# Optimization experiments

Measured on AMD Instinct MI355X. Metric: run time of the kernel, lower is better.

## Reference

```python
import jax, jax.numpy as jnp
import numpy as np

N_TOKEN = 392
POS_WEIGHT = 1.0
LOSS_WEIGHT = 1.0


def _cam_map(logits, w_proj, xf, shape):
    # logits: (B, K_cls); w_proj: (K_cls, C); xf: (B, C, N)
    B, T, H, W = shape
    top_cls = jnp.argmax(logits, axis=1)                 # sort desc -> [0] == argmax
    w_top = w_proj[top_cls]                              # (B, C) gather top-class weight row
    row = jnp.einsum('bc,bcn->bn', w_top, xf)            # (B, N) per-sample CAM scores
    mn = row.min(axis=1, keepdims=True)
    mx = row.max(axis=1, keepdims=True)
    rown = (row - mn) / (mx - mn)                        # min-max normalize
    vals, idxs = jax.lax.top_k(rown, N_TOKEN)            # (B, 392)
    hw = H * W
    ti = idxs // hw
    hi = (idxs % hw) // W
    wi = idxs % W
    bi = jnp.broadcast_to(jnp.arange(B)[:, None], idxs.shape)
    cam = jnp.zeros((B, T, H, W), rown.dtype).at[bi, ti, hi, wi].set(vals)
    return cam


def _forward(x, pred_v_logits, pred_n_logits, w_proj_v, w_proj_n,
             conv_w, conv_b, score_w, score_b):
    B, C, T, H, W = x.shape
    xf = x.reshape(B, C, T * H * W)
    cam_v = _cam_map(pred_v_logits, w_proj_v, xf, (B, T, H, W))
    cam_n = _cam_map(pred_n_logits, w_proj_n, xf, (B, T, H, W))
    cam_gt = jnp.maximum(cam_v, cam_n)                   # torch.where(v > n, v, n)
    cam_gt = jax.lax.stop_gradient(cam_gt)               # original builds it from numpy + .detach()

    dn = ('NCDHW', 'OIDHW', 'NCDHW')
    h1 = jax.nn.relu(
        jax.lax.conv_general_dilated(x, conv_w, (1, 1, 1),
                                     [(0, 0), (1, 1), (1, 1)],
                                     dimension_numbers=dn)
        + conv_b[None, :, None, None, None])
    logits = (jax.lax.conv_general_dilated(h1, score_w, (1, 1, 1),
                                           [(0, 0), (0, 0), (0, 0)],
                                           dimension_numbers=dn)
              + score_b[None, :, None, None, None])      # (B,1,T,H,W)

    xcam = logits[:, 0].reshape(B * T, H * W)
    y = cam_gt.reshape(B * T, H * W)
    # BCEWithLogitsLoss(pos_weight) mean
    bce = -(POS_WEIGHT * y * jax.nn.log_sigmoid(xcam)
            + (1.0 - y) * jax.nn.log_sigmoid(-xcam))
    return LOSS_WEIGHT * bce.mean()


def setup_inputs() -> dict:
    key = jax.random.key(0)
    ks = jax.random.split(key, 8)
    B, C, T, H, W = 64, 256, 32, 7, 7
    Kv, Kn, D = 97, 300, 512
    x = jax.random.normal(ks[0], (B, C, T, H, W), jnp.float32)
    pred_v_logits = jax.random.normal(ks[1], (B, Kv), jnp.float32)
    pred_n_logits = jax.random.normal(ks[2], (B, Kn), jnp.float32)
    w_proj_v = jax.random.normal(ks[3], (Kv, C), jnp.float32) / np.sqrt(C)
    w_proj_n = jax.random.normal(ks[4], (Kn, C), jnp.float32) / np.sqrt(C)
    conv_w = jax.random.normal(ks[5], (D, C, 1, 3, 3), jnp.float32) / np.sqrt(C * 9)
    conv_b = jnp.zeros((D,), jnp.float32)
    score_w = jax.random.normal(ks[6], (1, D, 1, 1, 1), jnp.float32) / np.sqrt(D)
    score_b = jnp.zeros((1,), jnp.float32)
    return {"x": x, "pred_v_logits": pred_v_logits, "pred_n_logits": pred_n_logits,
            "w_proj_v": w_proj_v, "w_proj_n": w_proj_n,
            "conv_w": conv_w, "conv_b": conv_b,
            "score_w": score_w, "score_b": score_b}


def reference(x, pred_v_logits, pred_n_logits, w_proj_v, w_proj_n,
              conv_w, conv_b, score_w, score_b):
    return _forward(x, pred_v_logits, pred_n_logits, w_proj_v, w_proj_n,
                    conv_w, conv_b, score_w, score_b)
```

## Files before the change

### kernel.cpp

```cpp
#include <hip/hip_runtime.h>
#include <hip/hip_bf16.h>
#include <math.h>

#define BB 64
#define CC 256
#define TT 32
#define HH 7
#define WW 7
#define HW 49
#define NN 1568
#define KV 97
#define KN 300
#define DD 512
#define NTOK 392
#define TOTAL (BB*TT*HW)
#define BCAP 256

typedef float f32x4 __attribute__((ext_vector_type(4)));
typedef short bf16x8 __attribute__((ext_vector_type(8)));

#define GLDS(g, l) __builtin_amdgcn_global_load_lds(                          \
    (const __attribute__((address_space(1))) void*)(g),                       \
    (__attribute__((address_space(3))) void*)(l), 16, 0, 0)

__global__ __launch_bounds__(256) void k_tr(
        const float* __restrict__ x, __hip_bfloat16* __restrict__ xp,
        const float* __restrict__ cw, __hip_bfloat16* __restrict__ wb,
        int* __restrict__ counter) {
    __shared__ float xs[392 * 33];
    int bid = blockIdx.x;
    int tid = threadIdx.x;
    if (bid == 0 && tid == 0) *counter = 0;

    {
        int base = bid * 576;
        #pragma unroll
        for (int r = 0; r < 3; ++r) {
            int o = base + r * 256 + tid;
            if (o < base + 576) {
                int kk = o / (DD * CC);
                int rem = o - kk * (DD * CC);
                int d = rem >> 8, c = rem & 255;
                wb[o] = __float2bfloat16(cw[(d * CC + c) * 9 + kk]);
            }
        }
    }

    int b  = bid >> 5;
    int cc = (bid >> 2) & 7;
    int tc = bid & 3;
    int c0 = cc << 5;
    int t0 = tc << 3;

    const float* xbase = x + ((size_t)((b * CC + c0) * TT + t0)) * HW;
    const float4* xb4 = (const float4*)xbase;
    for (int base = 0; base < 3072; base += 1024) {
        float4 v[4]; int li[4];
        #pragma unroll
        for (int j = 0; j < 4; ++j) {
            int idx = base + j * 256 + tid;
            v[j] = xb4[idx];
            int ch = idx / 98, o4 = idx - ch * 98;
            li[j] = (o4 * 4) * 33 + ch;
        }
        #pragma unroll
        for (int j = 0; j < 4; ++j) {
            xs[li[j]     ] = v[j].x;
            xs[li[j] + 33] = v[j].y;
            xs[li[j] + 66] = v[j].z;
            xs[li[j] + 99] = v[j].w;
        }
    }
    {
        int idx = 3072 + tid;
        if (idx < 3136) {
            float4 v = xb4[idx];
            int ch = idx / 98, o4 = idx - ch * 98;
            int li = (o4 * 4) * 33 + ch;
            xs[li] = v.x; xs[li + 33] = v.y; xs[li + 66] = v.z; xs[li + 99] = v.w;
        }
    }
    __syncthreads();

    __hip_bfloat16* xpb = xp + ((size_t)(b * TT + t0) * 81) * 256 + c0;
    for (int u = tid; u < 2592; u += 256) {
        int pos = u >> 2, cq = u & 3;
        int tt = pos / 81, p = pos - tt * 81;
        int hh = p / 9, ww = p - (p / 9) * 9;
        bool inb = (hh >= 1 && hh <= 7 && ww >= 1 && ww <= 7);
        const float* row = xs + (tt * 49 + (hh - 1) * 7 + (ww - 1)) * 33 + cq * 8;
        bf16x8 pack;
        #pragma unroll
        for (int j = 0; j < 8; ++j) {
            float v = inb ? row[j] : 0.f;
            __hip_bfloat16 bv = __float2bfloat16(v);
            pack[j] = *reinterpret_cast<short*>(&bv);
        }
        *reinterpret_cast<bf16x8*>(xpb + (size_t)(tt * 81 + p) * 256 + cq * 8) = pack;
    }
}

__device__ __forceinline__ int binof(float v) {
    int i = (int)(v * 1024.f);
    return i < 0 ? 0 : (i > 1023 ? 1023 : i);
}

__device__ void cam_block(int b, int tid, char* smem,
                          const float* __restrict__ x,
                          const float* __restrict__ pv, const float* __restrict__ pn,
                          const float* __restrict__ wpv, const float* __restrict__ wpn,
                          float* __restrict__ cam) {
    float* rv = (float*)smem;
    float* rn = (float*)(smem + 6272);
    int* h = (int*)(smem + 12544);
    int* tsum = (int*)(smem + 16640);
    float* lval_v = (float*)(smem + 17664);
    int* lidx_v = (int*)(smem + 18688);
    float* lval_n = (float*)(smem + 19712);
    int* lidx_n = (int*)(smem + 20736);
    float* wred = (float*)(smem + 21760);
    int* sc = (int*)(smem + 21824);
    float* wvs = (float*)(smem + 21888);
    float* wns = (float*)(smem + 22912);
    int* cls2 = (int*)(smem + 23936);

    int lane = tid & 63;
    if (tid < 128) {
        int head = tid >> 6;
        const float* r = head ? (pn + b * KN) : (pv + b * KV);
        int K = head ? KN : KV;
        float best = -1e30f; int bi = 0x7fffffff;
        for (int k = lane; k < K; k += 64) {
            float v = r[k];
            if (v > best || (v == best && k < bi)) { best = v; bi = k; }
        }
        #pragma unroll
        for (int off = 32; off >= 1; off >>= 1) {
            float ov = __shfl_xor(best, off);
            int oi = __shfl_xor(bi, off);
            if (ov > best || (ov == best && oi < bi)) { best = ov; bi = oi; }
        }
        if (lane == 0) cls2[head] = bi;
    }
    __syncthreads();
    wvs[tid] = wpv[cls2[0] * CC + tid];
    wns[tid] = wpn[cls2[1] * CC + tid];
    __syncthreads();

    {
        const f32x4* xb4 = (const f32x4*)(x + (size_t)b * CC * NN);
        bool two = tid < (392 - 256);
        f32x4 av0 = {0.f,0.f,0.f,0.f}, an0 = {0.f,0.f,0.f,0.f};
        f32x4 av1 = {0.f,0.f,0.f,0.f}, an1 = {0.f,0.f,0.f,0.f};
        for (int c = 0; c < CC; ++c) {
            float wv = wvs[c], wn = wns[c];
            const f32x4* rowc = xb4 + (size_t)c * 392;
            f32x4 u0 = rowc[tid];
            #pragma unroll
            for (int r = 0; r < 4; ++r) {
                av0[r] = fmaf(wv, u0[r], av0[r]);
                an0[r] = fmaf(wn, u0[r], an0[r]);
            }
            if (two) {
                f32x4 u1 = rowc[tid + 256];
                #pragma unroll
                for (int r = 0; r < 4; ++r) {
                    av1[r] = fmaf(wv, u1[r], av1[r]);
                    an1[r] = fmaf(wn, u1[r], an1[r]);
                }
            }
        }
        *reinterpret_cast<f32x4*>(rv + 4 * tid) = av0;
        *reinterpret_cast<f32x4*>(rn + 4 * tid) = an0;
        if (two) {
            *reinterpret_cast<f32x4*>(rv + 4 * (tid + 256)) = av1;
            *reinterpret_cast<f32x4*>(rn + 4 * (tid + 256)) = an1;
        }
    }
    __syncthreads();

    float mnv = 1e30f, mxv = -1e30f, mnn = 1e30f, mxn = -1e30f;
    for (int n = tid; n < NN; n += 256) {
        float v = rv[n]; mnv = fminf(mnv, v); mxv = fmaxf(mxv, v);
        float u = rn[n]; mnn = fminf(mnn, u); mxn = fmaxf(mxn, u);
    }
    #pragma unroll
    for (int off = 32; off >= 1; off >>= 1) {
        mnv = fminf(mnv, __shfl_xor(mnv, off));
        mxv = fmaxf(mxv, __shfl_xor(mxv, off));
        mnn = fminf(mnn, __shfl_xor(mnn, off));
        mxn = fmaxf(mxn, __shfl_xor(mxn, off));
    }
    if ((tid & 63) == 0) {
        int wid = tid >> 6;
        wred[wid * 4 + 0] = mnv; wred[wid * 4 + 1] = mxv;
        wred[wid * 4 + 2] = mnn; wred[wid * 4 + 3] = mxn;
    }
    if (tid == 0) { sc[0] = 0; sc[1] = 0; }
    __syncthreads();
    mnv = fminf(fminf(wred[0], wred[4]), fminf(wred[8], wred[12]));
    mxv = fmaxf(fmaxf(wred[1], wred[5]), fmaxf(wred[9], wred[13]));
    mnn = fminf(fminf(wred[2], wred[6]), fminf(wred[10], wred[14]));
    mxn = fmaxf(fmaxf(wred[3], wred[7]), fmaxf(wred[11], wred[15]));
    float iv = 1.f / (mxv - mnv), inn = 1.f / (mxn - mnn);

    for (int n = tid; n < NN; n += 256) {
        rv[n] = (rv[n] - mnv) * iv;
        rn[n] = (rn[n] - mnn) * inn;
    }
    for (int i = tid; i < 1024; i += 256) h[i] = 0;
    __syncthreads();
    for (int n = tid; n < NN; n += 256) {
        atomicAdd(&h[binof(rv[n])], 1);
        atomicAdd(&h[binof(rn[n])], 1 << 16);
    }
    __syncthreads();

    int h0 = h[4 * tid], h1 = h[4 * tid + 1], h2 = h[4 * tid + 2], h3 = h[4 * tid + 3];
    tsum[tid] = h0 + h1 + h2 + h3;
    __syncthreads();
    for (int off = 1; off < 256; off <<= 1) {
        int add = (tid + off < 256) ? tsum[tid + off] : 0;
        __syncthreads();
        tsum[tid] += add;
        __syncthreads();
    }
    {
        int scur = tsum[tid];
        int hk[4] = {h0, h1, h2, h3};
        #pragma unroll
        for (int k = 0; k < 4; ++k) {
            int snext = scur - hk[k];
            int scv = scur & 0xffff, ncv = snext & 0xffff;
            int sh = scur >> 16, nh = snext >> 16;
            if (scv >= NTOK && ncv < NTOK) { sc[2] = 4 * tid + k; sc[3] = ncv; }
            if (sh >= NTOK && nh < NTOK) { sc[4] = 4 * tid + k; sc[5] = nh; }
            scur = snext;
        }
    }
    __syncthreads();
    int bsv = sc[2], abv = sc[3], bsn = sc[4], abn = sc[5];

    for (int n = tid; n < NN; n += 256) {
        float v = rv[n]; int bv = binof(v);
        if (bv < bsv) rv[n] = 0.f;
        else if (bv == bsv) {
            int s = atomicAdd(&sc[0], 1);
            if (s < BCAP) { lval_v[s] = v; lidx_v[s] = n; }
        }
        float u = rn[n]; int bu = binof(u);
        if (bu < bsn) rn[n] = 0.f;
        else if (bu == bsn) {
            int s = atomicAdd(&sc[1], 1);
            if (s < BCAP) { lval_n[s] = u; lidx_n[s] = n; }
        }
    }
    __syncthreads();
    int Lv = sc[0] < BCAP ? sc[0] : BCAP;
    int Ln = sc[1] < BCAP ? sc[1] : BCAP;
    for (int i = tid; i < Lv; i += 256) {
        float vi = lval_v[i]; int ni = lidx_v[i]; int r = 0;
        for (int j = 0; j < Lv; ++j) {
            float vj = lval_v[j]; int nj = lidx_v[j];
            r += (vj > vi || (vj == vi && nj < ni)) ? 1 : 0;
        }
        rv[ni] = (r < NTOK - abv) ? vi : 0.f;
    }
    for (int i = tid; i < Ln; i += 256) {
        float vi = lval_n[i]; int ni = lidx_n[i]; int r = 0;
        for (int j = 0; j < Ln; ++j) {
            float vj = lval_n[j]; int nj = lidx_n[j];
            r += (vj > vi || (vj == vi && nj < ni)) ? 1 : 0;
        }
        rn[ni] = (r < NTOK - abn) ? vi : 0.f;
    }
    __syncthreads();
    for (int n = tid; n < NN; n += 256) cam[b * NN + n] = fmaxf(rv[n], rn[n]);
}

__global__ __launch_bounds__(256, 3) void k_gemm(
        const __hip_bfloat16* __restrict__ xp, const __hip_bfloat16* __restrict__ wb,
        const float* __restrict__ convb, const float* __restrict__ scorew,
        float* __restrict__ pl,
        const float* __restrict__ x,
        const float* __restrict__ pv, const float* __restrict__ pn,
        const float* __restrict__ wpv, const float* __restrict__ wpn,
        float* __restrict__ cam) {
    __shared__ char smem[32768];
    int tid = threadIdx.x;
    int bid = blockIdx.x;
    if (bid < 64) { cam_block(bid, tid, smem, x, pv, pn, wpv, wpn, cam); return; }
    char* As = smem;
    char* Bs = smem + 16384;
    int gid = bid - 64;
    int xcd = gid & 7;
    int local = gid >> 3;
    int mtile = xcd * 98 + (local >> 2);
    int nblk = local & 3;
    int m0 = mtile * 128;
    int n0 = nblk * 128;
    int lane = tid & 63, wv = tid >> 6;
    int wm = wv >> 1, wn = wv & 1;
    int ln = lane & 15, qd = lane >> 4;

    int rrow = tid >> 3;
    int segst = ((tid & 7) ^ (rrow & 7)) * 8;
    int bt_[4], hh_[4], ww_[4];
    const __hip_bfloat16* bptr[4];
    #pragma unroll
    for (int j = 0; j < 4; ++j) {
        int m = m0 + j * 32 + rrow;
        int bt = m / HW, q = m - bt * HW;
        bt_[j] = bt; hh_[j] = q / WW; ww_[j] = q - (q / WW) * WW;
        bptr[j] = wb + (size_t)(n0 + j * 32 + rrow) * 256 + segst;
    }

    int swz = ln & 7;
    int offk[2] = {((0 + qd) ^ swz) * 16, ((4 + qd) ^ swz) * 16};

    f32x4 acc[4][4];
    #pragma unroll
    for (int i = 0; i < 4; ++i)
        #pragma unroll
        for (int j = 0; j < 4; ++j) acc[i][j] = (f32x4){0.f, 0.f, 0.f, 0.f};

    for (int kk = 0; kk < 9; ++kk) {
        int kh = kk / 3, kw = kk - (kk / 3) * 3;
        const __hip_bfloat16* aptr[4];
        #pragma unroll
        for (int j = 0; j < 4; ++j)
            aptr[j] = xp + ((size_t)bt_[j] * 81 + (hh_[j] + kh) * 9 + (ww_[j] + kw)) * 256 + segst;
        const size_t boff = (size_t)kk * (DD * 256);
        #pragma unroll
        for (int c0 = 0; c0 < 256; c0 += 64) {
            __syncthreads();
            #pragma unroll
            for (int j = 0; j < 4; ++j) {
                GLDS(aptr[j] + c0, As + j * 4096 + tid * 16);
                GLDS(bptr[j] + boff + c0, Bs + j * 4096 + tid * 16);
            }
            __syncthreads();
            #pragma unroll
            for (int k2 = 0; k2 < 2; ++k2) {
                bf16x8 af[4], bfr[4];
                #pragma unroll
                for (int i = 0; i < 4; ++i)
                    af[i] = *(const bf16x8*)(As + (wm * 64 + i * 16 + ln) * 128 + offk[k2]);
                #pragma unroll
                for (int j = 0; j < 4; ++j)
                    bfr[j] = *(const bf16x8*)(Bs + (wn * 64 + j * 16 + ln) * 128 + offk[k2]);
                #pragma unroll
                for (int i = 0; i < 4; ++i)
                    #pragma unroll
                    for (int j = 0; j < 4; ++j)
                        acc[i][j] = __builtin_amdgcn_mfma_f32_16x16x32_bf16(af[i], bfr[j], acc[i][j], 0, 0, 0);
            }
        }
    }

    float swr[4], cbr[4];
    #pragma unroll
    for (int j = 0; j < 4; ++j) {
        int n = n0 + wn * 64 + j * 16 + ln;
        swr[j] = scorew[n];
        cbr[j] = convb[n];
    }
    float* dst = pl + (size_t)(nblk * 2 + wn) * TOTAL;
    #pragma unroll
    for (int i = 0; i < 4; ++i) {
        #pragma unroll
        for (int r = 0; r < 4; ++r) {
            float v = 0.f;
            #pragma unroll
            for (int j = 0; j < 4; ++j) {
                float h1 = acc[i][j][r] + cbr[j];
                h1 = h1 > 0.f ? h1 : 0.f;
                v = fmaf(swr[j], h1, v);
            }
            v += __shfl_xor(v, 1);
            v += __shfl_xor(v, 2);
            v += __shfl_xor(v, 4);
            v += __shfl_xor(v, 8);
            if (ln == 0)
                dst[m0 + wm * 64 + i * 16 + qd * 4 + r] = v;
        }
    }
}

__global__ __launch_bounds__(256) void k_bce(
        const float* __restrict__ pl, const float* __restrict__ cam,
        const float* __restrict__ sb, float* __restrict__ part,
        int* __restrict__ counter, float* __restrict__ out) {
    __shared__ float sbuf[256];
    __shared__ int isLast;
    int tid = threadIdx.x;
    int m = blockIdx.x * 256 + tid;
    float l = sb[0];
    #pragma unroll
    for (int s = 0; s < 8; ++s) l += pl[(size_t)s * TOTAL + m];
    float y = cam[m];
    float v = fmaxf(l, 0.f) - l * y + log1pf(expf(-fabsf(l)));
    sbuf[tid] = v; __syncthreads();
    for (int k = 128; k > 0; k >>= 1) {
        if (tid < k) sbuf[tid] += sbuf[tid + k];
        __syncthreads();
    }
    if (tid == 0) {
        part[blockIdx.x] = sbuf[0];
        __threadfence();
        int d = atomicAdd(counter, 1);
        isLast = (d == 391);
    }
    __syncthreads();
    if (isLast) {
        float s = 0.f;
        for (int i = tid; i < 392; i += 256) s += part[i];
        sbuf[tid] = s; __syncthreads();
        for (int k = 128; k > 0; k >>= 1) {
            if (tid < k) sbuf[tid] += sbuf[tid + k];
            __syncthreads();
        }
        if (tid == 0) out[0] = sbuf[0] * (1.0f / (float)TOTAL);
    }
}

extern "C" void kernel_launch(void* const* d_in, const int* in_sizes, int n_in,
                              void* d_out, int out_size, void* d_ws, size_t ws_size,
                              hipStream_t stream) {
    const float* x   = (const float*)d_in[0];
    const float* pv  = (const float*)d_in[1];
    const float* pn  = (const float*)d_in[2];
    const float* wpv = (const float*)d_in[3];
    const float* wpn = (const float*)d_in[4];
    const float* cw  = (const float*)d_in[5];
    const float* cb  = (const float*)d_in[6];
    const float* sw  = (const float*)d_in[7];
    const float* sb  = (const float*)d_in[8];

    char* w8 = (char*)d_ws;
    __hip_bfloat16* xp  = (__hip_bfloat16*)w8;
    __hip_bfloat16* wb  = (__hip_bfloat16*)(w8 + 84934656);
    float* pl      = (float*)(w8 + 87293952);
    float* cam     = (float*)(w8 + 90505216);
    float* part    = (float*)(w8 + 90906624);
    int*   counter = (int*)(w8 + 90908192);

    k_tr<<<2048, 256, 0, stream>>>(x, xp, cw, wb, counter);
    k_gemm<<<64 + 3136, 256, 0, stream>>>(xp, wb, cb, sw, pl,
                                          x, pv, pn, wpv, wpn, cam);
    k_bce<<<392, 256, 0, stream>>>(pl, cam, sb, part, counter, (float*)d_out);
}
```

Baseline: 411.6 us.

## Double-buffer LDS tiles to overlap global loads with MFMA compute

Restructures the conv-GEMM main loop into 36 flattened stages that use two 32KB LDS buffers. The next stage's global_load_lds is issued before computing on the current buffer, and partial vmcnt waits let the loads overlap the MFMA work. LDS doubles to 64KB and launch bounds drop to 2 blocks per SM, so occupancy falls in exchange for the overlap. It also relies on hand-placed s_barrier and waitcnt assembly, which may be fragile.

```diff
diff --git a/kernel.cpp b/kernel.cpp
--- a/kernel.cpp
+++ b/kernel.cpp
@@ -278,7 +278,7 @@
     for (int n = tid; n < NN; n += 256) cam[b * NN + n] = fmaxf(rv[n], rn[n]);
 }
 
-__global__ __launch_bounds__(256, 3) void k_gemm(
+__global__ __launch_bounds__(256, 2) void k_gemm(
         const __hip_bfloat16* __restrict__ xp, const __hip_bfloat16* __restrict__ wb,
         const float* __restrict__ convb, const float* __restrict__ scorew,
         float* __restrict__ pl,
@@ -286,12 +286,10 @@
         const float* __restrict__ pv, const float* __restrict__ pn,
         const float* __restrict__ wpv, const float* __restrict__ wpn,
         float* __restrict__ cam) {
-    __shared__ char smem[32768];
+    __shared__ char smem[65536];
     int tid = threadIdx.x;
     int bid = blockIdx.x;
     if (bid < 64) { cam_block(bid, tid, smem, x, pv, pn, wpv, wpn, cam); return; }
-    char* As = smem;
-    char* Bs = smem + 16384;
     int gid = bid - 64;
     int xcd = gid & 7;
     int local = gid >> 3;
@@ -324,37 +322,49 @@
         #pragma unroll
         for (int j = 0; j < 4; ++j) acc[i][j] = (f32x4){0.f, 0.f, 0.f, 0.f};
 
-    for (int kk = 0; kk < 9; ++kk) {
-        int kh = kk / 3, kw = kk - (kk / 3) * 3;
-        const __hip_bfloat16* aptr[4];
-        #pragma unroll
-        for (int j = 0; j < 4; ++j)
-            aptr[j] = xp + ((size_t)bt_[j] * 81 + (hh_[j] + kh) * 9 + (ww_[j] + kw)) * 256 + segst;
-        const size_t boff = (size_t)kk * (DD * 256);
-        #pragma unroll
-        for (int c0 = 0; c0 < 256; c0 += 64) {
-            __syncthreads();
+    auto STAGE = [&](int s, int wbo) {
+        int kk = s >> 2;
+        int kh = kk / 3, kw = kk - kh * 3;
+        int c0 = (s & 3) << 6;
+        const size_t boff = (size_t)kk * (DD * 256) + c0;
+        #pragma unroll
+        for (int j = 0; j < 4; ++j) {
+            const __hip_bfloat16* ap = xp
+                + ((size_t)bt_[j] * 81 + (hh_[j] + kh) * 9 + (ww_[j] + kw)) * 256
+                + segst + c0;
+            GLDS(ap, smem + wbo + j * 4096 + tid * 16);
+            GLDS(bptr[j] + boff, smem + wbo + 16384 + j * 4096 + tid * 16);
+        }
+    };
+
+    STAGE(0, 0);
+    #pragma unroll 2
+    for (int s = 0; s < 36; ++s) {
+        int rb = (s & 1) << 15;
+        asm volatile("s_barrier" ::: "memory");
+        if (s < 35) {
+            STAGE(s + 1, ((s + 1) & 1) << 15);
+            asm volatile("s_waitcnt vmcnt(8)" ::: "memory");
+        } else {
+            asm volatile("s_waitcnt vmcnt(0)" ::: "memory");
+        }
+        asm volatile("s_barrier" ::: "memory");
+        const char* Asr = smem + rb;
+        const char* Bsr = smem + rb + 16384;
+        #pragma unroll
+        for (int k2 = 0; k2 < 2; ++k2) {
+            bf16x8 af[4], bfr[4];
             #pragma unroll
-            for (int j = 0; j < 4; ++j) {
-                GLDS(aptr[j] + c0, As + j * 4096 + tid * 16);
-                GLDS(bptr[j] + boff + c0, Bs + j * 4096 + tid * 16);
-            }
-            __syncthreads();
+            for (int i = 0; i < 4; ++i)
+                af[i] = *(const bf16x8*)(Asr + (wm * 64 + i * 16 + ln) * 128 + offk[k2]);
             #pragma unroll
-            for (int k2 = 0; k2 < 2; ++k2) {
-                bf16x8 af[4], bfr[4];
-                #pragma unroll
-                for (int i = 0; i < 4; ++i)
-                    af[i] = *(const bf16x8*)(As + (wm * 64 + i * 16 + ln) * 128 + offk[k2]);
+            for (int j = 0; j < 4; ++j)
+                bfr[j] = *(const bf16x8*)(Bsr + (wn * 64 + j * 16 + ln) * 128 + offk[k2]);
+            #pragma unroll
+            for (int i = 0; i < 4; ++i)
                 #pragma unroll
                 for (int j = 0; j < 4; ++j)
-                    bfr[j] = *(const bf16x8*)(Bs + (wn * 64 + j * 16 + ln) * 128 + offk[k2]);
-                #pragma unroll
-                for (int i = 0; i < 4; ++i)
-                    #pragma unroll
-                    for (int j = 0; j < 4; ++j)
-                        acc[i][j] = __builtin_amdgcn_mfma_f32_16x16x32_bf16(af[i], bfr[j], acc[i][j], 0, 0, 0);
-            }
+                    acc[i][j] = __builtin_amdgcn_mfma_f32_16x16x32_bf16(af[i], bfr[j], acc[i][j], 0, 0, 0);
         }
     }
 
```

Measured after the change: 430.6 us. 4.6% more time.

## Restructure padded-transpose kernel to cover all channels per block with bf16 staging

Applied to the files above, without the earlier changes.

The transpose/pad kernel now gives each block all 256 channels for two time steps instead of 32 channels by 8 time steps, and halves the grid. Each thread loads its own channel's contiguous float2 run and converts to bf16 before writing to LDS. The LDS tile shrinks and the padded output is written as fully contiguous 16-byte stores per position row. The weight-conversion loop is widened to match the smaller grid. The cost is that the global loads are now strided across threads, since each lane reads a separate channel row. Coalescing then relies on cache reuse across loop iterations.

```diff
diff --git a/kernel.cpp b/kernel.cpp
--- a/kernel.cpp
+++ b/kernel.cpp
@@ -23,21 +23,21 @@
     (const __attribute__((address_space(1))) void*)(g),                       \
     (__attribute__((address_space(3))) void*)(l), 16, 0, 0)
 
-__global__ __launch_bounds__(256) void k_tr(
+__global__ __launch_bounds__(256, 3) void k_tr(
         const float* __restrict__ x, __hip_bfloat16* __restrict__ xp,
         const float* __restrict__ cw, __hip_bfloat16* __restrict__ wb,
         int* __restrict__ counter) {
-    __shared__ float xs[392 * 33];
+    __shared__ unsigned short xs[98 * 256];
     int bid = blockIdx.x;
     int tid = threadIdx.x;
     if (bid == 0 && tid == 0) *counter = 0;
 
     {
-        int base = bid * 576;
-        #pragma unroll
-        for (int r = 0; r < 3; ++r) {
+        int base = bid * 1152;
+        #pragma unroll
+        for (int r = 0; r < 5; ++r) {
             int o = base + r * 256 + tid;
-            if (o < base + 576) {
+            if (o < base + 1152) {
                 int kk = o / (DD * CC);
                 int rem = o - kk * (DD * CC);
                 int d = rem >> 8, c = rem & 255;
@@ -46,57 +46,46 @@
         }
     }
 
-    int b  = bid >> 5;
-    int cc = (bid >> 2) & 7;
-    int tc = bid & 3;
-    int c0 = cc << 5;
-    int t0 = tc << 3;
-
-    const float* xbase = x + ((size_t)((b * CC + c0) * TT + t0)) * HW;
-    const float4* xb4 = (const float4*)xbase;
-    for (int base = 0; base < 3072; base += 1024) {
-        float4 v[4]; int li[4];
-        #pragma unroll
-        for (int j = 0; j < 4; ++j) {
-            int idx = base + j * 256 + tid;
-            v[j] = xb4[idx];
-            int ch = idx / 98, o4 = idx - ch * 98;
-            li[j] = (o4 * 4) * 33 + ch;
-        }
-        #pragma unroll
-        for (int j = 0; j < 4; ++j) {
-            xs[li[j]     ] = v[j].x;
-            xs[li[j] + 33] = v[j].y;
-            xs[li[j] + 66] = v[j].z;
-            xs[li[j] + 99] = v[j].w;
+    int b  = bid >> 4;
+    int tp = bid & 15;
+    int t0 = tp << 1;
+
+    const float2* src = (const float2*)(x + ((size_t)(b * CC + tid) * TT + t0) * HW);
+    #pragma unroll 1
+    for (int r = 0; r < 6; ++r) {
+        float2 v[8];
+        #pragma unroll
+        for (int j = 0; j < 8; ++j) v[j] = src[r * 8 + j];
+        #pragma unroll
+        for (int j = 0; j < 8; ++j) {
+            int q = (r * 8 + j) * 2;
+            __hip_bfloat16 b0 = __float2bfloat16(v[j].x);
+            __hip_bfloat16 b1 = __float2bfloat16(v[j].y);
+            xs[q * 256 + tid] = *reinterpret_cast<unsigned short*>(&b0);
+            xs[(q + 1) * 256 + tid] = *reinterpret_cast<unsigned short*>(&b1);
         }
     }
     {
-        int idx = 3072 + tid;
-        if (idx < 3136) {
-            float4 v = xb4[idx];
-            int ch = idx / 98, o4 = idx - ch * 98;
-            int li = (o4 * 4) * 33 + ch;
-            xs[li] = v.x; xs[li + 33] = v.y; xs[li + 66] = v.z; xs[li + 99] = v.w;
-        }
-    }
-    __syncthreads();
-
-    __hip_bfloat16* xpb = xp + ((size_t)(b * TT + t0) * 81) * 256 + c0;
-    for (int u = tid; u < 2592; u += 256) {
-        int pos = u >> 2, cq = u & 3;
-        int tt = pos / 81, p = pos - tt * 81;
+        float2 v = src[48];
+        __hip_bfloat16 b0 = __float2bfloat16(v.x);
+        __hip_bfloat16 b1 = __float2bfloat16(v.y);
+        xs[96 * 256 + tid] = *reinterpret_cast<unsigned short*>(&b0);
+        xs[97 * 256 + tid] = *reinterpret_cast<unsigned short*>(&b1);
+    }
+    __syncthreads();
+
+    __hip_bfloat16* xpb = xp + (size_t)(b * TT + t0) * 81 * 256;
+    const bf16x8 zero = (bf16x8){0, 0, 0, 0, 0, 0, 0, 0};
+    for (int u = tid; u < 5184; u += 256) {
+        int pos = u >> 5, c0 = (u & 31) * 8;
+        int f = pos / 81, p = pos - f * 81;
         int hh = p / 9, ww = p - (p / 9) * 9;
-        bool inb = (hh >= 1 && hh <= 7 && ww >= 1 && ww <= 7);
-        const float* row = xs + (tt * 49 + (hh - 1) * 7 + (ww - 1)) * 33 + cq * 8;
-        bf16x8 pack;
-        #pragma unroll
-        for (int j = 0; j < 8; ++j) {
-            float v = inb ? row[j] : 0.f;
-            __hip_bfloat16 bv = __float2bfloat16(v);
-            pack[j] = *reinterpret_cast<short*>(&bv);
-        }
-        *reinterpret_cast<bf16x8*>(xpb + (size_t)(tt * 81 + p) * 256 + cq * 8) = pack;
+        bf16x8 val = zero;
+        if (hh >= 1 && hh <= 7 && ww >= 1 && ww <= 7) {
+            int q = f * 49 + (hh - 1) * 7 + (ww - 1);
+            val = *reinterpret_cast<const bf16x8*>(xs + q * 256 + c0);
+        }
+        *reinterpret_cast<bf16x8*>(xpb + (size_t)u * 8) = val;
     }
 }
 
@@ -445,7 +434,7 @@
     float* part    = (float*)(w8 + 90906624);
     int*   counter = (int*)(w8 + 90908192);
 
-    k_tr<<<2048, 256, 0, stream>>>(x, xp, cw, wb, counter);
+    k_tr<<<1024, 256, 0, stream>>>(x, xp, cw, wb, counter);
     k_gemm<<<64 + 3136, 256, 0, stream>>>(xp, wb, cb, sw, pl,
                                           x, pv, pn, wpv, wpn, cam);
     k_bce<<<392, 256, 0, stream>>>(pl, cam, sb, part, counter, (float*)d_out);
```

Result: slower. 432.7 us (+5.1%).

## Drop padded halo from bf16 activation copy and redirect halo loads to zero buffer

Applied to the files above, without the earlier changes.

The transpose kernel now writes the bf16 channels-last activation without the 9x9 zero-padded halo, which cuts the intermediate buffer from 81 to 49 positions per frame and shrinks write traffic. The implicit-GEMM kernel computes the halo condition per row and points halo loads at a small zeroed buffer that the transpose kernel initializes. Separately, the CAM dot-product loop is unrolled by four channels so more global loads are in flight at once. The extra per-row index arithmetic is small, and the zero buffer holds 64 float4 (1024 bytes), so each thread's 16-byte load at zb+segst must stay inside it.

```diff
diff --git a/kernel.cpp b/kernel.cpp
--- a/kernel.cpp
+++ b/kernel.cpp
@@ -26,11 +26,14 @@
 __global__ __launch_bounds__(256) void k_tr(
         const float* __restrict__ x, __hip_bfloat16* __restrict__ xp,
         const float* __restrict__ cw, __hip_bfloat16* __restrict__ wb,
-        int* __restrict__ counter) {
+        int* __restrict__ counter, float* __restrict__ zbuf) {
     __shared__ float xs[392 * 33];
     int bid = blockIdx.x;
     int tid = threadIdx.x;
-    if (bid == 0 && tid == 0) *counter = 0;
+    if (bid == 0) {
+        if (tid == 0) *counter = 0;
+        if (tid < 64) reinterpret_cast<float4*>(zbuf)[tid] = (float4){0.f, 0.f, 0.f, 0.f};
+    }
 
     {
         int base = bid * 576;
@@ -82,21 +85,17 @@
     }
     __syncthreads();
 
-    __hip_bfloat16* xpb = xp + ((size_t)(b * TT + t0) * 81) * 256 + c0;
-    for (int u = tid; u < 2592; u += 256) {
+    __hip_bfloat16* xpb = xp + ((size_t)(b * TT + t0) * HW) * 256 + c0;
+    for (int u = tid; u < 1568; u += 256) {
         int pos = u >> 2, cq = u & 3;
-        int tt = pos / 81, p = pos - tt * 81;
-        int hh = p / 9, ww = p - (p / 9) * 9;
-        bool inb = (hh >= 1 && hh <= 7 && ww >= 1 && ww <= 7);
-        const float* row = xs + (tt * 49 + (hh - 1) * 7 + (ww - 1)) * 33 + cq * 8;
+        const float* row = xs + pos * 33 + cq * 8;
         bf16x8 pack;
         #pragma unroll
         for (int j = 0; j < 8; ++j) {
-            float v = inb ? row[j] : 0.f;
-            __hip_bfloat16 bv = __float2bfloat16(v);
+            __hip_bfloat16 bv = __float2bfloat16(row[j]);
             pack[j] = *reinterpret_cast<short*>(&bv);
         }
-        *reinterpret_cast<bf16x8*>(xpb + (size_t)(tt * 81 + p) * 256 + cq * 8) = pack;
+        *reinterpret_cast<bf16x8*>(xpb + (size_t)pos * 256 + cq * 8) = pack;
     }
 }
 
@@ -148,25 +147,32 @@
     __syncthreads();
 
     {
-        const f32x4* xb4 = (const f32x4*)(x + (size_t)b * CC * NN);
+        const f32x4* p0 = (const f32x4*)(x + (size_t)b * CC * NN) + tid;
         bool two = tid < (392 - 256);
         f32x4 av0 = {0.f,0.f,0.f,0.f}, an0 = {0.f,0.f,0.f,0.f};
         f32x4 av1 = {0.f,0.f,0.f,0.f}, an1 = {0.f,0.f,0.f,0.f};
-        for (int c = 0; c < CC; ++c) {
-            float wv = wvs[c], wn = wns[c];
-            const f32x4* rowc = xb4 + (size_t)c * 392;
-            f32x4 u0 = rowc[tid];
+        for (int c = 0; c < CC; c += 4) {
+            f32x4 u0[4], u1[4];
             #pragma unroll
-            for (int r = 0; r < 4; ++r) {
-                av0[r] = fmaf(wv, u0[r], av0[r]);
-                an0[r] = fmaf(wn, u0[r], an0[r]);
-            }
+            for (int d = 0; d < 4; ++d) u0[d] = p0[(size_t)(c + d) * 392];
             if (two) {
-                f32x4 u1 = rowc[tid + 256];
+                #pragma unroll
+                for (int d = 0; d < 4; ++d) u1[d] = p0[(size_t)(c + d) * 392 + 256];
+            }
+            #pragma unroll
+            for (int d = 0; d < 4; ++d) {
+                float wv = wvs[c + d], wn = wns[c + d];
                 #pragma unroll
                 for (int r = 0; r < 4; ++r) {
-                    av1[r] = fmaf(wv, u1[r], av1[r]);
-                    an1[r] = fmaf(wn, u1[r], an1[r]);
+                    av0[r] = fmaf(wv, u0[d][r], av0[r]);
+                    an0[r] = fmaf(wn, u0[d][r], an0[r]);
+                }
+                if (two) {
+                    #pragma unroll
+                    for (int r = 0; r < 4; ++r) {
+                        av1[r] = fmaf(wv, u1[d][r], av1[r]);
+                        an1[r] = fmaf(wn, u1[d][r], an1[r]);
+                    }
                 }
             }
         }
@@ -285,7 +291,7 @@
         const float* __restrict__ x,
         const float* __restrict__ pv, const float* __restrict__ pn,
         const float* __restrict__ wpv, const float* __restrict__ wpn,
-        float* __restrict__ cam) {
+        float* __restrict__ cam, const __hip_bfloat16* __restrict__ zb) {
     __shared__ char smem[32768];
     int tid = threadIdx.x;
     int bid = blockIdx.x;
@@ -328,8 +334,12 @@
         int kh = kk / 3, kw = kk - (kk / 3) * 3;
         const __hip_bfloat16* aptr[4];
         #pragma unroll
-        for (int j = 0; j < 4; ++j)
-            aptr[j] = xp + ((size_t)bt_[j] * 81 + (hh_[j] + kh) * 9 + (ww_[j] + kw)) * 256 + segst;
+        for (int j = 0; j < 4; ++j) {
+            int ph = hh_[j] + kh, pw = ww_[j] + kw;
+            bool halo = (ph == 0) | (ph == 8) | (pw == 0) | (pw == 8);
+            aptr[j] = halo ? zb
+                : xp + ((size_t)bt_[j] * HW + (ph - 1) * 7 + (pw - 1)) * 256 + segst;
+        }
         const size_t boff = (size_t)kk * (DD * 256);
         #pragma unroll
         for (int c0 = 0; c0 < 256; c0 += 64) {
@@ -439,14 +449,16 @@
 
     char* w8 = (char*)d_ws;
     __hip_bfloat16* xp  = (__hip_bfloat16*)w8;
-    __hip_bfloat16* wb  = (__hip_bfloat16*)(w8 + 84934656);
-    float* pl      = (float*)(w8 + 87293952);
-    float* cam     = (float*)(w8 + 90505216);
-    float* part    = (float*)(w8 + 90906624);
-    int*   counter = (int*)(w8 + 90908192);
-
-    k_tr<<<2048, 256, 0, stream>>>(x, xp, cw, wb, counter);
+    __hip_bfloat16* wb  = (__hip_bfloat16*)(w8 + 51380224);
+    float* pl      = (float*)(w8 + 53739520);
+    float* cam     = (float*)(w8 + 56950784);
+    float* part    = (float*)(w8 + 57352192);
+    int*   counter = (int*)(w8 + 57353760);
+    float* zbuf    = (float*)(w8 + 57353776);
+
+    k_tr<<<2048, 256, 0, stream>>>(x, xp, cw, wb, counter, zbuf);
     k_gemm<<<64 + 3136, 256, 0, stream>>>(xp, wb, cb, sw, pl,
-                                          x, pv, pn, wpv, wpn, cam);
+                                          x, pv, pn, wpv, wpn, cam,
+                                          (const __hip_bfloat16*)zbuf);
     k_bce<<<392, 256, 0, stream>>>(pl, cam, sb, part, counter, (float*)d_out);
 }
```

Result: faster. 391.6 us (-4.9%).
